# Performance work log

Measured on AMD Instinct MI355X. Metric: run time of the kernel, lower is better.

The kernel has to match this reference:

```python
import jax, jax.numpy as jnp
import numpy as np

DIMENSIONS = 10000
NUM_LEVELS = 256
SIZE = 28
BATCH = 64
NUM_CLASSES = 10


def _bipolar(key, shape):
    # torchhd MAP hypervectors are random +/-1
    return jnp.where(jax.random.uniform(key, shape) > 0.5, 1.0, -1.0).astype(jnp.float32)


def setup_inputs() -> dict:
    key = jax.random.key(0)
    kx, kpx, kpy, kv, kw = jax.random.split(key, 5)
    # pixel intensities in [0, 1]
    x = jax.random.uniform(kx, (BATCH, SIZE, SIZE), dtype=jnp.float32)
    # position = hard_quantize(bundle(px, py)) with px, py random bipolar HVs
    px = _bipolar(kpx, (SIZE * SIZE, DIMENSIONS))
    py = _bipolar(kpy, (SIZE * SIZE, DIMENSIONS))
    position = jnp.where(px + py > 0, 1.0, -1.0).astype(jnp.float32)
    # Level embedding table (bipolar hypervectors per intensity level)
    level_weight = _bipolar(kv, (NUM_LEVELS, DIMENSIONS))
    # classify Linear weight (zero in original; small random here so output is non-trivial)
    classify_weight = jax.random.normal(kw, (NUM_CLASSES, DIMENSIONS), jnp.float32) * 0.01
    return {"x": x, "position": position, "level_weight": level_weight,
            "classify_weight": classify_weight}


def reference(x, position, level_weight, classify_weight):
    B = x.shape[0]
    xf = x.reshape(B, -1)                                   # [B, P] with P = size*size
    # torchhd Level: value in [0,1] -> round to one of NUM_LEVELS indices
    idx = jnp.clip(jnp.round(xf * (NUM_LEVELS - 1)), 0, NUM_LEVELS - 1).astype(jnp.int32)
    # bind: gather level HVs and elementwise-multiply with position HVs, then multiset-bundle (sum over P)
    bundled = jnp.einsum('bpd,pd->bd', level_weight[idx], position)  # [B, D]
    # hard_quantize: sign threshold (>0 -> 1, else -1)
    enc = jnp.where(bundled > 0, 1.0, -1.0).astype(x.dtype)
    # classify: Linear(DIMENSIONS, num_classes, bias=False)
    logit = enc @ classify_weight.T                          # [B, num_classes]
    return logit
```

## Files before the change

kernel.cpp:

```cpp
#include <hip/hip_runtime.h>
#include <stdint.h>

#define D      10000
#define WPR    313
#define NPIX   784
#define NB     64
#define NC     10

__global__ __launch_bounds__(320) void pack_kernel(const float* __restrict__ lev,
                                                   const float* __restrict__ pos,
                                                   uint32_t* __restrict__ Lp,
                                                   uint32_t* __restrict__ Pp,
                                                   float* __restrict__ out) {
    if (blockIdx.x == 0)
        for (int i = threadIdx.x; i < NB * NC; i += 320) out[i] = 0.0f;

    int row = blockIdx.x;
    const float* src; uint32_t* dst;
    if (row < 256) { src = lev + (size_t)row * D;        dst = Lp + row * WPR; }
    else           { src = pos + (size_t)(row - 256) * D; dst = Pp + (row - 256) * WPR; }

    int w = threadIdx.x;
    if (w >= WPR) return;
    const uint4* p4 = (const uint4*)((const uint32_t*)src + w * 32);
    uint32_t word = 0;
    if (w < WPR - 1) {
        #pragma unroll
        for (int k = 0; k < 8; ++k) {
            uint4 u = p4[k];
            word |= (u.x >> 31) << (4 * k)     | (u.y >> 31) << (4 * k + 1)
                  | (u.z >> 31) << (4 * k + 2) | (u.w >> 31) << (4 * k + 3);
        }
    } else {
        #pragma unroll
        for (int k = 0; k < 4; ++k) {
            uint4 u = p4[k];
            word |= (u.x >> 31) << (4 * k)     | (u.y >> 31) << (4 * k + 1)
                  | (u.z >> 31) << (4 * k + 2) | (u.w >> 31) << (4 * k + 3);
        }
    }
    dst[w] = word;
}

__global__ __launch_bounds__(512) void fused_kernel(const float* __restrict__ x,
                                                    const uint32_t* __restrict__ Lp,
                                                    const uint32_t* __restrict__ Pp,
                                                    const float* __restrict__ cw,
                                                    float* __restrict__ out) {
    int tid = threadIdx.x;
    int b = blockIdx.y;
    int bx = blockIdx.x;
    int t = tid >> 6, lane = tid & 63;
    int w32 = lane & 31, h = lane >> 5;
    int w = bx * 32 + w32;
    int wc = w < WPR ? w : WPR - 1;

    __shared__ int idxs[NPIX];
    __shared__ uint32_t part[16][8][36];
    __shared__ float red[8][NC];

    for (int i = tid; i < NPIX; i += 512) {
        float xv = x[b * NPIX + i];
        int v = (int)rintf(xv * 255.0f);
        v = v < 0 ? 0 : (v > 255 ? 255 : v);
        idxs[i] = v * WPR;
    }
    __syncthreads();

    int cc = 2 * t + h;
    int p0 = cc * 49;
    uint32_t s0 = 0, s1 = 0, s2 = 0, s3 = 0, s4 = 0, s5 = 0;
    const uint32_t* pp = Pp + (size_t)p0 * WPR + wc;
    #pragma unroll 7
    for (int i = 0; i < 49; ++i) {
        int ro = idxs[p0 + i];
        uint32_t c = Lp[ro + wc] ^ pp[(size_t)i * WPR];
        uint32_t tt;
        tt = s0 & c; s0 ^= c; c = tt;
        tt = s1 & c; s1 ^= c; c = tt;
        tt = s2 & c; s2 ^= c; c = tt;
        tt = s3 & c; s3 ^= c; c = tt;
        tt = s4 & c; s4 ^= c; c = tt;
        s5 ^= c;
    }

    #pragma unroll
    for (int q = 0; q < 8; ++q) {
        uint32_t wordv = 0;
        #pragma unroll
        for (int r = 0; r < 4; ++r) {
            int j = q * 4 + r;
            uint32_t cnt = ((s0 >> j) & 1u)        | (((s1 >> j) & 1u) << 1)
                         | (((s2 >> j) & 1u) << 2) | (((s3 >> j) & 1u) << 3)
                         | (((s4 >> j) & 1u) << 4) | (((s5 >> j) & 1u) << 5);
            wordv |= cnt << (8 * r);
        }
        part[cc][q][w32] = wordv;
    }
    __syncthreads();

    float acc[NC];
    #pragma unroll
    for (int c = 0; c < NC; ++c) acc[c] = 0.0f;

    if (tid < 256) {
        int rw = tid >> 3, q = tid & 7;
        int ww = bx * 32 + rw;
        int d0 = ww * 32 + q * 4;
        if (ww < WPR && d0 + 3 < D) {
            uint32_t se = 0, so = 0;
            #pragma unroll
            for (int k = 0; k < 16; ++k) {
                uint32_t u = part[k][q][rw];
                se += u & 0x00FF00FFu;
                so += (u >> 8) & 0x00FF00FFu;
            }
            int c0 = se & 0xFFFFu, c1 = so & 0xFFFFu;
            int c2 = se >> 16,     c3 = so >> 16;
            float e0 = (2 * c0 < NPIX) ? 1.0f : -1.0f;
            float e1 = (2 * c1 < NPIX) ? 1.0f : -1.0f;
            float e2 = (2 * c2 < NPIX) ? 1.0f : -1.0f;
            float e3 = (2 * c3 < NPIX) ? 1.0f : -1.0f;
            #pragma unroll
            for (int c = 0; c < NC; ++c) {
                const float4 v = *(const float4*)(cw + (size_t)c * D + d0);
                acc[c] = fmaf(e0, v.x, fmaf(e1, v.y, fmaf(e2, v.z, fmaf(e3, v.w, acc[c]))));
            }
        }
    }

    #pragma unroll
    for (int c = 0; c < NC; ++c) {
        float v = acc[c];
        #pragma unroll
        for (int off = 32; off > 0; off >>= 1) v += __shfl_down(v, off, 64);
        if (lane == 0) red[t][c] = v;
    }
    __syncthreads();
    if (tid < NC) {
        float s = red[0][tid];
        #pragma unroll
        for (int t2 = 1; t2 < 8; ++t2) s += red[t2][tid];
        atomicAdd(&out[b * NC + tid], s);
    }
}

extern "C" void kernel_launch(void* const* d_in, const int* in_sizes, int n_in,
                              void* d_out, int out_size, void* d_ws, size_t ws_size,
                              hipStream_t stream) {
    const float* x   = (const float*)d_in[0];
    const float* pos = (const float*)d_in[1];
    const float* lev = (const float*)d_in[2];
    const float* cw  = (const float*)d_in[3];
    float* out = (float*)d_out;

    uint32_t* Lp = (uint32_t*)d_ws;
    uint32_t* Pp = Lp + 256 * WPR;

    pack_kernel<<<256 + NPIX, 320, 0, stream>>>(lev, pos, Lp, Pp, out);
    dim3 g(10, NB);
    fused_kernel<<<g, 512, 0, stream>>>(x, Lp, Pp, cw, out);
}
```

Before: 106.8 us.

## Merge pack and fused kernels into one cooperative kernel with grid sync

Replaces the two launches (bit-pack kernel, then fused bind/bundle/classify kernel) with a single cooperative launch of 640 blocks. Packing is spread over all threads, followed by a grid-wide barrier before the main computation. This removes one kernel launch and the inter-kernel gap, at the cost of a grid sync and a cooperative launch, with a fallback to the old path if the launch fails.

```diff
diff --git a/kernel.cpp b/kernel.cpp
--- a/kernel.cpp
+++ b/kernel.cpp
@@ -1,4 +1,5 @@
 #include <hip/hip_runtime.h>
+#include <hip/hip_cooperative_groups.h>
 #include <stdint.h>
 
 #define D      10000
@@ -6,6 +7,10 @@
 #define NPIX   784
 #define NB     64
 #define NC     10
+#define TOTW   (1040 * WPR)
+
+namespace cg = cooperative_groups;
+
 
 __global__ __launch_bounds__(320) void pack_kernel(const float* __restrict__ lev,
                                                    const float* __restrict__ pos,
@@ -145,6 +150,144 @@
     }
 }
 
+__global__ __launch_bounds__(512, 6) void mega_kernel(const float* __restrict__ x,
+                                                      const float* __restrict__ lev,
+                                                      const float* __restrict__ pos,
+                                                      const float* __restrict__ cw,
+                                                      uint32_t* __restrict__ Lp,
+                                                      uint32_t* __restrict__ Pp,
+                                                      float* __restrict__ out) {
+    int tid = threadIdx.x;
+
+    if (blockIdx.x == 0)
+        for (int i = tid; i < NB * NC; i += 512) out[i] = 0.0f;
+
+    unsigned gtid = blockIdx.x * 512u + (unsigned)tid;
+    if (gtid < TOTW) {
+        unsigned row = gtid / WPR;
+        int w = (int)(gtid - row * WPR);
+        const float* src; uint32_t* dst;
+        if (row < 256) { src = lev + (size_t)row * D;         dst = Lp + row * WPR; }
+        else           { src = pos + (size_t)(row - 256) * D; dst = Pp + (row - 256) * WPR; }
+        const uint4* p4 = (const uint4*)((const uint32_t*)src + w * 32);
+        uint32_t word = 0;
+        if (w < WPR - 1) {
+            #pragma unroll
+            for (int k = 0; k < 8; ++k) {
+                uint4 u = p4[k];
+                word |= (u.x >> 31) << (4 * k)     | (u.y >> 31) << (4 * k + 1)
+                      | (u.z >> 31) << (4 * k + 2) | (u.w >> 31) << (4 * k + 3);
+            }
+        } else {
+            #pragma unroll
+            for (int k = 0; k < 4; ++k) {
+                uint4 u = p4[k];
+                word |= (u.x >> 31) << (4 * k)     | (u.y >> 31) << (4 * k + 1)
+                      | (u.z >> 31) << (4 * k + 2) | (u.w >> 31) << (4 * k + 3);
+            }
+        }
+        dst[w] = word;
+    }
+
+    __threadfence();
+    cg::this_grid().sync();
+
+    int b = blockIdx.x & 63, bx = blockIdx.x >> 6;
+    int t = tid >> 6, lane = tid & 63;
+    int w32 = lane & 31, h = lane >> 5;
+    int w = bx * 32 + w32;
+    int wc = w < WPR ? w : WPR - 1;
+
+    __shared__ int idxs[NPIX];
+    __shared__ uint32_t part[16][8][36];
+    __shared__ float red[8][NC];
+
+    for (int i = tid; i < NPIX; i += 512) {
+        float xv = x[b * NPIX + i];
+        int v = (int)rintf(xv * 255.0f);
+        v = v < 0 ? 0 : (v > 255 ? 255 : v);
+        idxs[i] = v * WPR;
+    }
+    __syncthreads();
+
+    int cc = 2 * t + h;
+    int p0 = cc * 49;
+    uint32_t s0 = 0, s1 = 0, s2 = 0, s3 = 0, s4 = 0, s5 = 0;
+    const uint32_t* pp = Pp + (size_t)p0 * WPR + wc;
+    #pragma unroll 7
+    for (int i = 0; i < 49; ++i) {
+        int ro = idxs[p0 + i];
+        uint32_t c = Lp[ro + wc] ^ pp[(size_t)i * WPR];
+        uint32_t tt;
+        tt = s0 & c; s0 ^= c; c = tt;
+        tt = s1 & c; s1 ^= c; c = tt;
+        tt = s2 & c; s2 ^= c; c = tt;
+        tt = s3 & c; s3 ^= c; c = tt;
+        tt = s4 & c; s4 ^= c; c = tt;
+        s5 ^= c;
+    }
+
+    #pragma unroll
+    for (int q = 0; q < 8; ++q) {
+        uint32_t wordv = 0;
+        #pragma unroll
+        for (int r = 0; r < 4; ++r) {
+            int j = q * 4 + r;
+            uint32_t cnt = ((s0 >> j) & 1u)        | (((s1 >> j) & 1u) << 1)
+                         | (((s2 >> j) & 1u) << 2) | (((s3 >> j) & 1u) << 3)
+                         | (((s4 >> j) & 1u) << 4) | (((s5 >> j) & 1u) << 5);
+            wordv |= cnt << (8 * r);
+        }
+        part[cc][q][w32] = wordv;
+    }
+    __syncthreads();
+
+    float acc[NC];
+    #pragma unroll
+    for (int c = 0; c < NC; ++c) acc[c] = 0.0f;
+
+    if (tid < 256) {
+        int rw = tid >> 3, q = tid & 7;
+        int ww = bx * 32 + rw;
+        int d0 = ww * 32 + q * 4;
+        if (ww < WPR && d0 + 3 < D) {
+            uint32_t se = 0, so = 0;
+            #pragma unroll
+            for (int k = 0; k < 16; ++k) {
+                uint32_t u = part[k][q][rw];
+                se += u & 0x00FF00FFu;
+                so += (u >> 8) & 0x00FF00FFu;
+            }
+            int c0 = se & 0xFFFFu, c1 = so & 0xFFFFu;
+            int c2 = se >> 16,     c3 = so >> 16;
+            float e0 = (2 * c0 < NPIX) ? 1.0f : -1.0f;
+            float e1 = (2 * c1 < NPIX) ? 1.0f : -1.0f;
+            float e2 = (2 * c2 < NPIX) ? 1.0f : -1.0f;
+            float e3 = (2 * c3 < NPIX) ? 1.0f : -1.0f;
+            #pragma unroll
+            for (int c = 0; c < NC; ++c) {
+                const float4 v = *(const float4*)(cw + (size_t)c * D + d0);
+                acc[c] = fmaf(e0, v.x, fmaf(e1, v.y, fmaf(e2, v.z, fmaf(e3, v.w, acc[c]))));
+            }
+        }
+    }
+
+    #pragma unroll
+    for (int c = 0; c < NC; ++c) {
+        float v = acc[c];
+        #pragma unroll
+        for (int off = 32; off > 0; off >>= 1) v += __shfl_down(v, off, 64);
+        if (lane == 0) red[t][c] = v;
+    }
+    __syncthreads();
+    if (tid < NC) {
+        float s = red[0][tid];
+        #pragma unroll
+        for (int t2 = 1; t2 < 8; ++t2) s += red[t2][tid];
+        atomicAdd(&out[b * NC + tid], s);
+    }
+}
+
 extern "C" void kernel_launch(void* const* d_in, const int* in_sizes, int n_in,
                               void* d_out, int out_size, void* d_ws, size_t ws_size,
                               hipStream_t stream) {
@@ -157,7 +300,14 @@
     uint32_t* Lp = (uint32_t*)d_ws;
     uint32_t* Pp = Lp + 256 * WPR;
 
-    pack_kernel<<<256 + NPIX, 320, 0, stream>>>(lev, pos, Lp, Pp, out);
-    dim3 g(10, NB);
-    fused_kernel<<<g, 512, 0, stream>>>(x, Lp, Pp, cw, out);
+    void* args[] = { (void*)&x, (void*)&lev, (void*)&pos, (void*)&cw,
+                     (void*)&Lp, (void*)&Pp, (void*)&out };
+    hipError_t err = hipLaunchCooperativeKernel((const void*)mega_kernel,
+                                                dim3(640), dim3(512),
+                                                args, 0, stream);
+    if (err != hipSuccess) {
+        pack_kernel<<<256 + NPIX, 320, 0, stream>>>(lev, pos, Lp, Pp, out);
+        dim3 g(10, NB);
+        fused_kernel<<<g, 512, 0, stream>>>(x, Lp, Pp, cw, out);
+    }
 }
```

After: 303.2 us. 184% more time.
